# Optimization experiments

Measured on AMD Instinct MI355X. Metric: run time of the kernel, lower is better.

## Reference

```python
import jax, jax.numpy as jnp
import numpy as np

N_NODES = 100000
N_EDGES = 3200000
DIM = 64
N_DRUGS_Q = 8192


def setup_inputs() -> dict:
    key = jax.random.key(0)
    k1, k2, k3, k4, k5 = jax.random.split(key, 5)
    emb = jax.random.normal(k1, (N_NODES, DIM), dtype=jnp.float32) * 0.1
    # normalized-adjacency-like positive edge weights
    edge_vals = jax.random.uniform(k2, (N_EDGES,), dtype=jnp.float32) / 32.0
    edge_row = jax.random.randint(k3, (N_EDGES,), 0, N_NODES, dtype=jnp.int32)
    edge_col = jax.random.randint(k4, (N_EDGES,), 0, N_NODES, dtype=jnp.int32)
    drugs = jax.random.randint(k5, (N_DRUGS_Q,), 0, N_NODES, dtype=jnp.int32)
    return {"emb": emb, "edge_vals": edge_vals, "edge_row": edge_row,
            "edge_col": edge_col, "drugs": drugs}


def _spmm(edge_vals, edge_row, edge_col, x, n_nodes):
    # y[r] = sum_{e: row[e]==r} vals[e] * x[col[e]]   (sparse.mm(G, x))
    gathered = edge_vals[:, None] * x[edge_col]  # [E, D]
    return jax.ops.segment_sum(gathered, edge_row, num_segments=n_nodes)


def reference(emb, edge_vals, edge_row, edge_col, drugs):
    n = emb.shape[0]

    def ode_block(x):
        # single euler step over a unit time interval: x + dt * G @ x, dt = 1
        return x + _spmm(edge_vals, edge_row, edge_col, x, n)

    e0 = emb
    d1 = ode_block(e0) - e0
    d2 = ode_block(d1) - d1
    d3 = ode_block(d2) - d2
    d4 = ode_block(d3) - d3
    # stack([e0,d1,d2,d3,d4], dim=1).mean(dim=1)
    light_out = (e0 + d1 + d2 + d3 + d4) / 5.0
    drugs_emb = light_out[drugs]           # [B, D]
    gamma = jnp.sum(drugs_emb * drugs_emb, axis=1)  # [B]
    return gamma
```

## Files before the change

### kernel.cpp

```cpp
#include <hip/hip_runtime.h>


typedef unsigned int u32;

#define RB 256
#define RB_SHIFT 8
#define NBMAX 512
#define CHUNK 16384
#define SCAN_CHUNK 4096
#define NXCD 8
#define VSC 7.62939453125e-06f


__global__ __launch_bounds__(512) void countA_kernel(const int* __restrict__ row,
                                                     int* __restrict__ cmat,
                                                     int E, int nb, int nchunks) {
    __shared__ int lcnt[NBMAX];
    int t = threadIdx.x, c = blockIdx.x;
    int s = c * CHUNK, e = min(s + CHUNK, E);
    for (int i = t; i < nb; i += 512) lcnt[i] = 0;
    __syncthreads();
    for (int i = s + t * 4; i < e; i += 512 * 4) {
        if (i + 3 < e) {
            int4 r4 = *(const int4*)(row + i);
            atomicAdd(&lcnt[r4.x >> RB_SHIFT], 1);
            atomicAdd(&lcnt[r4.y >> RB_SHIFT], 1);
            atomicAdd(&lcnt[r4.z >> RB_SHIFT], 1);
            atomicAdd(&lcnt[r4.w >> RB_SHIFT], 1);
        } else {
            for (int k = i; k < e; ++k) atomicAdd(&lcnt[row[k] >> RB_SHIFT], 1);
        }
    }
    __syncthreads();
    for (int b = t; b < nb; b += 512)
        cmat[(size_t)b * nchunks + c] = lcnt[b];
}

__global__ __launch_bounds__(256) void scanA_kernel(const int* __restrict__ data,
                                                    int* __restrict__ partial, int M) {
    __shared__ int sdata[256];
    int t = threadIdx.x;
    int base = blockIdx.x * SCAN_CHUNK;
    int sum = 0;
#pragma unroll
    for (int j = 0; j < 16; ++j) {
        int idx = base + j * 256 + t;
        if (idx < M) sum += data[idx];
    }
    sdata[t] = sum;
    __syncthreads();
    for (int d = 128; d > 0; d >>= 1) {
        if (t < d) sdata[t] += sdata[t + d];
        __syncthreads();
    }
    if (t == 0) partial[blockIdx.x] = sdata[0];
}

__global__ __launch_bounds__(256) void scanB_kernel(int* __restrict__ partial, int nblk) {
    __shared__ int sdata[256];
    int t = threadIdx.x;
    int v = (t < nblk) ? partial[t] : 0;
    sdata[t] = v;
    __syncthreads();
    for (int d = 1; d < 256; d <<= 1) {
        int tmp = (t >= d) ? sdata[t - d] : 0;
        __syncthreads();
        sdata[t] += tmp;
        __syncthreads();
    }
    if (t < nblk) partial[t] = sdata[t] - v;
}

__global__ __launch_bounds__(256) void scanC_kernel(int* __restrict__ data,
                                                    const int* __restrict__ partial, int M) {
    __shared__ int sdata[256];
    int t = threadIdx.x;
    int base = blockIdx.x * SCAN_CHUNK;
    int v[16];
    int sum = 0;
#pragma unroll
    for (int j = 0; j < 16; ++j) {
        int idx = base + t * 16 + j;
        v[j] = (idx < M) ? data[idx] : 0;
        sum += v[j];
    }
    sdata[t] = sum;
    __syncthreads();
    for (int d = 1; d < 256; d <<= 1) {
        int tmp = (t >= d) ? sdata[t - d] : 0;
        __syncthreads();
        sdata[t] += tmp;
        __syncthreads();
    }
    int excl = sdata[t] - sum + partial[blockIdx.x];
#pragma unroll
    for (int j = 0; j < 16; ++j) {
        int idx = base + t * 16 + j;
        if (idx < M) data[idx] = excl;
        excl += v[j];
    }
}

__global__ __launch_bounds__(256) void extract_boff_kernel(const int* __restrict__ cmat,
                                                           int* __restrict__ boff,
                                                           int nb, int nchunks, int E) {
    int b = blockIdx.x * 256 + threadIdx.x;
    if (b < nb) boff[b] = cmat[(size_t)b * nchunks];
    if (b == nb) boff[nb] = E;
}

static __device__ inline int chunk_swizzle(int b, int nchunks) {
    int x = b & (NXCD - 1), idx = b >> 3;
    int q = nchunks >> 3, r = nchunks & (NXCD - 1);
    int base = (x < r) ? x * (q + 1) : r * (q + 1) + (x - r) * q;
    return base + idx;
}

__global__ __launch_bounds__(512) void part2_kernel(const int* __restrict__ row,
                                                    const int* __restrict__ col,
                                                    const float* __restrict__ val,
                                                    const int* __restrict__ cmat,
                                                    int2* __restrict__ edges,
                                                    int E, int nb, int nchunks) {
    __shared__ int lcur[NBMAX];
    int t = threadIdx.x;
    int c = chunk_swizzle(blockIdx.x, nchunks);
    int s = c * CHUNK, e = min(s + CHUNK, E);
    for (int b = t; b < nb; b += 512)
        lcur[b] = cmat[(size_t)b * nchunks + c];
    __syncthreads();
    for (int i = s + t * 4; i < e; i += 512 * 4) {
        if (i + 3 < e) {
            int4   r4 = *(const int4*)(row + i);
            int4   c4 = *(const int4*)(col + i);
            float4 v4 = *(const float4*)(val + i);
            int lo0 = atomicAdd(&lcur[r4.x >> RB_SHIFT], 1);
            int lo1 = atomicAdd(&lcur[r4.y >> RB_SHIFT], 1);
            int lo2 = atomicAdd(&lcur[r4.z >> RB_SHIFT], 1);
            int lo3 = atomicAdd(&lcur[r4.w >> RB_SHIFT], 1);
            edges[lo0] = make_int2(((r4.x & (RB - 1)) << 20) | c4.x, __float_as_int(v4.x));
            edges[lo1] = make_int2(((r4.y & (RB - 1)) << 20) | c4.y, __float_as_int(v4.y));
            edges[lo2] = make_int2(((r4.z & (RB - 1)) << 20) | c4.z, __float_as_int(v4.z));
            edges[lo3] = make_int2(((r4.w & (RB - 1)) << 20) | c4.w, __float_as_int(v4.w));
        } else {
            for (int k = i; k < e; ++k) {
                int r = row[k];
                int lo = atomicAdd(&lcur[r >> RB_SHIFT], 1);
                edges[lo] = make_int2(((r & (RB - 1)) << 20) | col[k],
                                      __float_as_int(val[k]));
            }
        }
    }
}

__global__ __launch_bounds__(256) void bsort_kernel(const int* __restrict__ boff,
                                                    const int2* __restrict__ ein,
                                                    u32* __restrict__ eout,
                                                    int* __restrict__ off, int N) {
    __shared__ int rcnt[RB];
    __shared__ int rcur[RB];
    __shared__ int sscan[256];
    int b = blockIdx.x, t = threadIdx.x;
    int s = boff[b], e = boff[b + 1];
    rcnt[t] = 0;
    __syncthreads();
    for (int i = s + t; i < e; i += 256)
        atomicAdd(&rcnt[ein[i].x >> 20], 1);
    __syncthreads();
    int v = rcnt[t];
    sscan[t] = v;
    __syncthreads();
    for (int d = 1; d < 256; d <<= 1) {
        int tmp = (t >= d) ? sscan[t - d] : 0;
        __syncthreads();
        sscan[t] += tmp;
        __syncthreads();
    }
    int excl = sscan[t] - v;
    rcur[t] = excl;
    int idx = (b << RB_SHIFT) + t;
    if (idx <= N) off[idx] = s + excl;
    if (t == 255) {
        int idx2 = (b << RB_SHIFT) + 256;
        if (idx2 <= N) off[idx2] = e;
    }
    __syncthreads();
    for (int i = s + t; i < e; i += 256) {
        int2 m = ein[i];
        int pos = atomicAdd(&rcur[m.x >> 20], 1);
        float vv = __int_as_float(m.y);
        u32 q = (u32)fminf(vv * 131072.0f + 0.5f, 4095.0f);
        eout[s + pos] = (q << 20) | (u32)(m.x & 0xFFFFF);
    }
}


static __device__ inline u32 pk_bf16(float lo, float hi) {
    u32 a = __float_as_uint(lo), b = __float_as_uint(hi);
    a += 0x7fffu + ((a >> 16) & 1u);
    b += 0x7fffu + ((b >> 16) & 1u);
    return (a >> 16) | (b & 0xffff0000u);
}

__global__ __launch_bounds__(256) void cvt_kernel(const float* __restrict__ src,
                                                  u32* __restrict__ dst, int n32) {
    int idx = blockIdx.x * 256 + threadIdx.x;
    if (idx >= n32) return;
    float2 f = *(const float2*)(src + (size_t)idx * 2);
    dst[idx] = pk_bf16(f.x, f.y);
}

__global__ __launch_bounds__(256) void spmmh_kernel(const u32* __restrict__ xh,
                                                    u32* __restrict__ yh,
                                                    const int* __restrict__ off,
                                                    const u32* __restrict__ edges, int N) {
    int g = (blockIdx.x * 256 + threadIdx.x) >> 4;
    int l = threadIdx.x & 15;
    if (g >= N) return;
    int s = off[g], e = off[g + 1];
    float a0 = 0.f, a1 = 0.f, a2 = 0.f, a3 = 0.f;
#define ACC4(r, v)                                                    \
    do {                                                              \
        a0 += (v) * __uint_as_float((r).x << 16);                     \
        a1 += (v) * __uint_as_float((r).x & 0xffff0000u);             \
        a2 += (v) * __uint_as_float((r).y << 16);                     \
        a3 += (v) * __uint_as_float((r).y & 0xffff0000u);             \
    } while (0)

    int i = s;
    for (; i + 8 <= e; i += 8) {
        uint4 eA = *(const uint4*)(edges + i);
        uint4 eB = *(const uint4*)(edges + i + 4);
        uint2 r0 = *(const uint2*)(xh + (size_t)(eA.x & 0xFFFFFu) * 32 + l * 2);
        uint2 r1 = *(const uint2*)(xh + (size_t)(eA.y & 0xFFFFFu) * 32 + l * 2);
        uint2 r2 = *(const uint2*)(xh + (size_t)(eA.z & 0xFFFFFu) * 32 + l * 2);
        uint2 r3 = *(const uint2*)(xh + (size_t)(eA.w & 0xFFFFFu) * 32 + l * 2);
        uint2 r4 = *(const uint2*)(xh + (size_t)(eB.x & 0xFFFFFu) * 32 + l * 2);
        uint2 r5 = *(const uint2*)(xh + (size_t)(eB.y & 0xFFFFFu) * 32 + l * 2);
        uint2 r6 = *(const uint2*)(xh + (size_t)(eB.z & 0xFFFFFu) * 32 + l * 2);
        uint2 r7 = *(const uint2*)(xh + (size_t)(eB.w & 0xFFFFFu) * 32 + l * 2);
        ACC4(r0, (float)(eA.x >> 20) * VSC);
        ACC4(r1, (float)(eA.y >> 20) * VSC);
        ACC4(r2, (float)(eA.z >> 20) * VSC);
        ACC4(r3, (float)(eA.w >> 20) * VSC);
        ACC4(r4, (float)(eB.x >> 20) * VSC);
        ACC4(r5, (float)(eB.y >> 20) * VSC);
        ACC4(r6, (float)(eB.z >> 20) * VSC);
        ACC4(r7, (float)(eB.w >> 20) * VSC);
    }
    for (; i < e; ++i) {
        u32 m = edges[i];
        uint2 rv = *(const uint2*)(xh + (size_t)(m & 0xFFFFFu) * 32 + l * 2);
        ACC4(rv, (float)(m >> 20) * VSC);
    }
#undef ACC4
    uint2 out;
    out.x = pk_bf16(a0, a1);
    out.y = pk_bf16(a2, a3);
    *(uint2*)(yh + (size_t)g * 32 + l * 2) = out;
}

__global__ __launch_bounds__(256) void dspmm_kernel(const u32* __restrict__ xh,
                                                    float* __restrict__ sacc,
                                                    const int* __restrict__ off,
                                                    const u32* __restrict__ edges,
                                                    const int* __restrict__ drugs, int B) {
    int g = (blockIdx.x * 256 + threadIdx.x) >> 4;
    int l = threadIdx.x & 15;
    if (g >= B) return;
    int r = drugs[g];
    int s = off[r], e = off[r + 1];
    float a0 = 0.f, a1 = 0.f, a2 = 0.f, a3 = 0.f;
#define ACC4(r_, v)                                                   \
    do {                                                              \
        a0 += (v) * __uint_as_float((r_).x << 16);                    \
        a1 += (v) * __uint_as_float((r_).x & 0xffff0000u);            \
        a2 += (v) * __uint_as_float((r_).y << 16);                    \
        a3 += (v) * __uint_as_float((r_).y & 0xffff0000u);            \
    } while (0)
    int i = s;
    for (; i + 4 <= e; i += 4) {
        uint4 eA = *(const uint4*)(edges + i);
        uint2 r0 = *(const uint2*)(xh + (size_t)(eA.x & 0xFFFFFu) * 32 + l * 2);
        uint2 r1 = *(const uint2*)(xh + (size_t)(eA.y & 0xFFFFFu) * 32 + l * 2);
        uint2 r2 = *(const uint2*)(xh + (size_t)(eA.z & 0xFFFFFu) * 32 + l * 2);
        uint2 r3 = *(const uint2*)(xh + (size_t)(eA.w & 0xFFFFFu) * 32 + l * 2);
        ACC4(r0, (float)(eA.x >> 20) * VSC);
        ACC4(r1, (float)(eA.y >> 20) * VSC);
        ACC4(r2, (float)(eA.z >> 20) * VSC);
        ACC4(r3, (float)(eA.w >> 20) * VSC);
    }
    for (; i < e; ++i) {
        u32 m = edges[i];
        uint2 rv = *(const uint2*)(xh + (size_t)(m & 0xFFFFFu) * 32 + l * 2);
        ACC4(rv, (float)(m >> 20) * VSC);
    }
#undef ACC4
    float4* p = (float4*)(sacc + (size_t)g * 64 + l * 4);
    float4 cur = *p;
    cur.x += a0; cur.y += a1; cur.z += a2; cur.w += a3;
    *p = cur;
}


__global__ __launch_bounds__(256) void gather_init_kernel(float* __restrict__ sacc,
                                                          const float* __restrict__ src,
                                                          const int* __restrict__ drugs, int B) {
    int idx = blockIdx.x * 256 + threadIdx.x;
    if (idx >= B * 64) return;
    int i = idx >> 6, d = idx & 63;
    sacc[idx] = src[(size_t)drugs[i] * 64 + d];
}

__global__ __launch_bounds__(256) void gather_addh_kernel(float* __restrict__ sacc,
                                                          const u32* __restrict__ srch,
                                                          const int* __restrict__ drugs, int B) {
    int idx = blockIdx.x * 256 + threadIdx.x;
    if (idx >= B * 32) return;
    int i = idx >> 5, k = idx & 31;
    u32 u = srch[(size_t)drugs[i] * 32 + k];
    sacc[i * 64 + 2 * k]     += __uint_as_float(u << 16);
    sacc[i * 64 + 2 * k + 1] += __uint_as_float(u & 0xffff0000u);
}

__global__ __launch_bounds__(256) void gamma_kernel(const float* __restrict__ sacc,
                                                    float* __restrict__ out, int B) {
    int w = (blockIdx.x * 256 + threadIdx.x) >> 6;
    int lane = threadIdx.x & 63;
    if (w >= B) return;
    float v = sacc[(size_t)w * 64 + lane] * 0.2f;
    v = v * v;
    for (int o = 32; o > 0; o >>= 1) v += __shfl_down(v, o, 64);
    if (lane == 0) out[w] = v;
}

extern "C" void kernel_launch(void* const* d_in, const int* in_sizes, int n_in,
                              void* d_out, int out_size, void* d_ws, size_t ws_size,
                              hipStream_t stream) {
    (void)n_in; (void)ws_size; (void)out_size;
    const float* emb       = (const float*)d_in[0];
    const float* edge_vals = (const float*)d_in[1];
    const int*   edge_row  = (const int*)d_in[2];
    const int*   edge_col  = (const int*)d_in[3];
    const int*   drugs     = (const int*)d_in[4];
    int N = in_sizes[0] / 64;
    int E = in_sizes[1];
    int B = in_sizes[4];
    float* gamma_out = (float*)d_out;

    int nb = (N + RB - 1) >> RB_SHIFT;
    int nchunks = (E + CHUNK - 1) / CHUNK;
    int M = nb * nchunks;

    char* ws = (char*)d_ws;
    size_t o = 0;
    auto alloc = [&](size_t bytes) -> void* {
        o = (o + 255) & ~(size_t)255;
        void* p = ws + o;
        o += bytes;
        return p;
    };
    size_t ebytes8 = (size_t)E * 8;
    size_t ebytes4 = (size_t)E * 4;
    size_t hbytes  = (size_t)N * 32 * 4;
    int*   cmat    = (int*)alloc((size_t)M * 4);
    int*   partial = (int*)alloc(1024);
    int*   boff    = (int*)alloc((size_t)(nb + 1) * 4);
    int*   off     = (int*)alloc((size_t)(N + 1) * 4);
    char*  reg0    = (char*)alloc(ebytes8 > hbytes ? ebytes8 : hbytes);
    int2*  ein     = (int2*)reg0;
    u32*   embh    = (u32*)reg0;
    u32*   eout    = (u32*)alloc(ebytes4);
    u32*   bufHA   = (u32*)alloc(hbytes);
    u32*   bufHB   = (u32*)alloc(hbytes);
    float* sacc    = (float*)alloc((size_t)B * 64 * 4);

    countA_kernel<<<nchunks, 512, 0, stream>>>(edge_row, cmat, E, nb, nchunks);
    int nscan = (M + SCAN_CHUNK - 1) / SCAN_CHUNK;
    scanA_kernel<<<nscan, 256, 0, stream>>>(cmat, partial, M);
    scanB_kernel<<<1, 256, 0, stream>>>(partial, nscan);
    scanC_kernel<<<nscan, 256, 0, stream>>>(cmat, partial, M);
    extract_boff_kernel<<<(nb + 256) / 256, 256, 0, stream>>>(cmat, boff, nb, nchunks, E);
    part2_kernel<<<nchunks, 512, 0, stream>>>(edge_row, edge_col, edge_vals,
                                              cmat, ein, E, nb, nchunks);
    bsort_kernel<<<nb, 256, 0, stream>>>(boff, ein, eout, off, N);

    int n32 = N * 32;
    cvt_kernel<<<(n32 + 255) / 256, 256, 0, stream>>>(emb, embh, n32);

    int gatherGrid64 = (B * 64 + 255) / 256;
    int gatherGrid32 = (B * 32 + 255) / 256;
    gather_init_kernel<<<gatherGrid64, 256, 0, stream>>>(sacc, emb, drugs, B);

    int spmmGrid = ((size_t)N * 16 + 255) / 256;
    spmmh_kernel<<<spmmGrid, 256, 0, stream>>>(embh, bufHA, off, eout, N);
    gather_addh_kernel<<<gatherGrid32, 256, 0, stream>>>(sacc, bufHA, drugs, B);
    spmmh_kernel<<<spmmGrid, 256, 0, stream>>>(bufHA, bufHB, off, eout, N);
    gather_addh_kernel<<<gatherGrid32, 256, 0, stream>>>(sacc, bufHB, drugs, B);
    spmmh_kernel<<<spmmGrid, 256, 0, stream>>>(bufHB, bufHA, off, eout, N);
    gather_addh_kernel<<<gatherGrid32, 256, 0, stream>>>(sacc, bufHA, drugs, B);
    int dGrid = ((size_t)B * 16 + 255) / 256;
    dspmm_kernel<<<dGrid, 256, 0, stream>>>(bufHA, sacc, off, eout, drugs, B);

    gamma_kernel<<<(B + 3) / 4, 256, 0, stream>>>(sacc, gamma_out, B);
}
```

Measured before the change: 268.5 us.

## Fuse small kernels, halve partition chunk size, widen bucket-sort blocks

Folds the boff extraction into the scan kernel, merges the initial gather into the first gather-add, and fuses the final drug SpMM with the gamma reduction. Together these remove three kernel launches and one round trip of the accumulator through memory. It also halves the edge partition chunk, giving more blocks to count and partition but a larger count matrix to scan. The bucket sort now uses 512 threads per block. The added modulo per scanned element and the idle upper half of threads during the bucket-sort scan are small extra costs.

```diff
diff --git a/kernel.cpp b/kernel.cpp
--- a/kernel.cpp
+++ b/kernel.cpp
@@ -6,7 +6,7 @@
 #define RB 256
 #define RB_SHIFT 8
 #define NBMAX 512
-#define CHUNK 16384
+#define CHUNK 8192
 #define SCAN_CHUNK 4096
 #define NXCD 8
 #define VSC 7.62939453125e-06f
@@ -72,7 +72,9 @@
 }
 
 __global__ __launch_bounds__(256) void scanC_kernel(int* __restrict__ data,
-                                                    const int* __restrict__ partial, int M) {
+                                                    const int* __restrict__ partial,
+                                                    int* __restrict__ boff,
+                                                    int M, int nchunks, int nb, int E) {
     __shared__ int sdata[256];
     int t = threadIdx.x;
     int base = blockIdx.x * SCAN_CHUNK;
@@ -96,17 +98,13 @@
 #pragma unroll
     for (int j = 0; j < 16; ++j) {
         int idx = base + t * 16 + j;
-        if (idx < M) data[idx] = excl;
+        if (idx < M) {
+            data[idx] = excl;
+            if (idx % nchunks == 0) boff[idx / nchunks] = excl;
+        }
         excl += v[j];
     }
-}
-
-__global__ __launch_bounds__(256) void extract_boff_kernel(const int* __restrict__ cmat,
-                                                           int* __restrict__ boff,
-                                                           int nb, int nchunks, int E) {
-    int b = blockIdx.x * 256 + threadIdx.x;
-    if (b < nb) boff[b] = cmat[(size_t)b * nchunks];
-    if (b == nb) boff[nb] = E;
+    if (blockIdx.x == 0 && t == 0) boff[nb] = E;
 }
 
 static __device__ inline int chunk_swizzle(int b, int nchunks) {
@@ -153,7 +151,7 @@
     }
 }
 
-__global__ __launch_bounds__(256) void bsort_kernel(const int* __restrict__ boff,
+__global__ __launch_bounds__(512) void bsort_kernel(const int* __restrict__ boff,
                                                     const int2* __restrict__ ein,
                                                     u32* __restrict__ eout,
                                                     int* __restrict__ off, int N) {
@@ -162,30 +160,33 @@
     __shared__ int sscan[256];
     int b = blockIdx.x, t = threadIdx.x;
     int s = boff[b], e = boff[b + 1];
-    rcnt[t] = 0;
-    __syncthreads();
-    for (int i = s + t; i < e; i += 256)
+    if (t < 256) rcnt[t] = 0;
+    __syncthreads();
+    for (int i = s + t; i < e; i += 512)
         atomicAdd(&rcnt[ein[i].x >> 20], 1);
     __syncthreads();
-    int v = rcnt[t];
-    sscan[t] = v;
+    int v = 0;
+    if (t < 256) { v = rcnt[t]; sscan[t] = v; }
     __syncthreads();
     for (int d = 1; d < 256; d <<= 1) {
-        int tmp = (t >= d) ? sscan[t - d] : 0;
-        __syncthreads();
-        sscan[t] += tmp;
-        __syncthreads();
-    }
-    int excl = sscan[t] - v;
-    rcur[t] = excl;
-    int idx = (b << RB_SHIFT) + t;
-    if (idx <= N) off[idx] = s + excl;
-    if (t == 255) {
-        int idx2 = (b << RB_SHIFT) + 256;
-        if (idx2 <= N) off[idx2] = e;
-    }
-    __syncthreads();
-    for (int i = s + t; i < e; i += 256) {
+        int tmp = 0;
+        if (t < 256 && t >= d) tmp = sscan[t - d];
+        __syncthreads();
+        if (t < 256) sscan[t] += tmp;
+        __syncthreads();
+    }
+    if (t < 256) {
+        int excl = sscan[t] - v;
+        rcur[t] = excl;
+        int idx = (b << RB_SHIFT) + t;
+        if (idx <= N) off[idx] = s + excl;
+        if (t == 255) {
+            int idx2 = (b << RB_SHIFT) + 256;
+            if (idx2 <= N) off[idx2] = e;
+        }
+    }
+    __syncthreads();
+    for (int i = s + t; i < e; i += 512) {
         int2 m = ein[i];
         int pos = atomicAdd(&rcur[m.x >> 20], 1);
         float vv = __int_as_float(m.y);
@@ -260,11 +261,12 @@
     *(uint2*)(yh + (size_t)g * 32 + l * 2) = out;
 }
 
-__global__ __launch_bounds__(256) void dspmm_kernel(const u32* __restrict__ xh,
-                                                    float* __restrict__ sacc,
-                                                    const int* __restrict__ off,
-                                                    const u32* __restrict__ edges,
-                                                    const int* __restrict__ drugs, int B) {
+__global__ __launch_bounds__(256) void dspmm_gamma_kernel(const u32* __restrict__ xh,
+                                                          const float* __restrict__ sacc,
+                                                          const int* __restrict__ off,
+                                                          const u32* __restrict__ edges,
+                                                          const int* __restrict__ drugs,
+                                                          float* __restrict__ out, int B) {
     int g = (blockIdx.x * 256 + threadIdx.x) >> 4;
     int l = threadIdx.x & 15;
     if (g >= B) return;
@@ -296,20 +298,29 @@
         ACC4(rv, (float)(m >> 20) * VSC);
     }
 #undef ACC4
-    float4* p = (float4*)(sacc + (size_t)g * 64 + l * 4);
-    float4 cur = *p;
-    cur.x += a0; cur.y += a1; cur.z += a2; cur.w += a3;
-    *p = cur;
-}
-
-
-__global__ __launch_bounds__(256) void gather_init_kernel(float* __restrict__ sacc,
-                                                          const float* __restrict__ src,
-                                                          const int* __restrict__ drugs, int B) {
+    float4 cur = *(const float4*)(sacc + (size_t)g * 64 + l * 4);
+    float x0 = (cur.x + a0) * 0.2f;
+    float x1 = (cur.y + a1) * 0.2f;
+    float x2 = (cur.z + a2) * 0.2f;
+    float x3 = (cur.w + a3) * 0.2f;
+    float v = x0 * x0 + x1 * x1 + x2 * x2 + x3 * x3;
+    for (int o = 8; o > 0; o >>= 1) v += __shfl_down(v, o, 16);
+    if (l == 0) out[g] = v;
+}
+
+
+__global__ __launch_bounds__(256) void gather_init_addh_kernel(float* __restrict__ sacc,
+                                                               const float* __restrict__ emb,
+                                                               const u32* __restrict__ srch,
+                                                               const int* __restrict__ drugs, int B) {
     int idx = blockIdx.x * 256 + threadIdx.x;
-    if (idx >= B * 64) return;
-    int i = idx >> 6, d = idx & 63;
-    sacc[idx] = src[(size_t)drugs[i] * 64 + d];
+    if (idx >= B * 32) return;
+    int i = idx >> 5, k = idx & 31;
+    int r = drugs[i];
+    float2 f = *(const float2*)(emb + (size_t)r * 64 + 2 * k);
+    u32 u = srch[(size_t)r * 32 + k];
+    sacc[i * 64 + 2 * k]     = f.x + __uint_as_float(u << 16);
+    sacc[i * 64 + 2 * k + 1] = f.y + __uint_as_float(u & 0xffff0000u);
 }
 
 __global__ __launch_bounds__(256) void gather_addh_kernel(float* __restrict__ sacc,
@@ -321,17 +332,6 @@
     u32 u = srch[(size_t)drugs[i] * 32 + k];
     sacc[i * 64 + 2 * k]     += __uint_as_float(u << 16);
     sacc[i * 64 + 2 * k + 1] += __uint_as_float(u & 0xffff0000u);
-}
-
-__global__ __launch_bounds__(256) void gamma_kernel(const float* __restrict__ sacc,
-                                                    float* __restrict__ out, int B) {
-    int w = (blockIdx.x * 256 + threadIdx.x) >> 6;
-    int lane = threadIdx.x & 63;
-    if (w >= B) return;
-    float v = sacc[(size_t)w * 64 + lane] * 0.2f;
-    v = v * v;
-    for (int o = 32; o > 0; o >>= 1) v += __shfl_down(v, o, 64);
-    if (lane == 0) out[w] = v;
 }
 
 extern "C" void kernel_launch(void* const* d_in, const int* in_sizes, int n_in,
@@ -379,28 +379,24 @@
     int nscan = (M + SCAN_CHUNK - 1) / SCAN_CHUNK;
     scanA_kernel<<<nscan, 256, 0, stream>>>(cmat, partial, M);
     scanB_kernel<<<1, 256, 0, stream>>>(partial, nscan);
-    scanC_kernel<<<nscan, 256, 0, stream>>>(cmat, partial, M);
-    extract_boff_kernel<<<(nb + 256) / 256, 256, 0, stream>>>(cmat, boff, nb, nchunks, E);
+    scanC_kernel<<<nscan, 256, 0, stream>>>(cmat, partial, boff, M, nchunks, nb, E);
     part2_kernel<<<nchunks, 512, 0, stream>>>(edge_row, edge_col, edge_vals,
                                               cmat, ein, E, nb, nchunks);
-    bsort_kernel<<<nb, 256, 0, stream>>>(boff, ein, eout, off, N);
+    bsort_kernel<<<nb, 512, 0, stream>>>(boff, ein, eout, off, N);
 
     int n32 = N * 32;
     cvt_kernel<<<(n32 + 255) / 256, 256, 0, stream>>>(emb, embh, n32);
 
-    int gatherGrid64 = (B * 64 + 255) / 256;
     int gatherGrid32 = (B * 32 + 255) / 256;
-    gather_init_kernel<<<gatherGrid64, 256, 0, stream>>>(sacc, emb, drugs, B);
-
     int spmmGrid = ((size_t)N * 16 + 255) / 256;
+
     spmmh_kernel<<<spmmGrid, 256, 0, stream>>>(embh, bufHA, off, eout, N);
-    gather_addh_kernel<<<gatherGrid32, 256, 0, stream>>>(sacc, bufHA, drugs, B);
+    gather_init_addh_kernel<<<gatherGrid32, 256, 0, stream>>>(sacc, emb, bufHA, drugs, B);
     spmmh_kernel<<<spmmGrid, 256, 0, stream>>>(bufHA, bufHB, off, eout, N);
     gather_addh_kernel<<<gatherGrid32, 256, 0, stream>>>(sacc, bufHB, drugs, B);
     spmmh_kernel<<<spmmGrid, 256, 0, stream>>>(bufHB, bufHA, off, eout, N);
     gather_addh_kernel<<<gatherGrid32, 256, 0, stream>>>(sacc, bufHA, drugs, B);
     int dGrid = ((size_t)B * 16 + 255) / 256;
-    dspmm_kernel<<<dGrid, 256, 0, stream>>>(bufHA, sacc, off, eout, drugs, B);
-
-    gamma_kernel<<<(B + 3) / 4, 256, 0, stream>>>(sacc, gamma_out, B);
-}
+    dspmm_gamma_kernel<<<dGrid, 256, 0, stream>>>(bufHA, sacc, off, eout, drugs,
+                                                  gamma_out, B);
+}
```

After: 260.7 us. -2.9%, faster.
